# Performance work log

Hardware: AMD Instinct MI355X
Metric: run time of the kernel (lower is better)

## Reference

```python
import jax, jax.numpy as jnp
import numpy as np


def _rnn_scan(x_tbi, h0, Wih, Whh, bih, bhh):
    # x_tbi: [T,B,I], h0: [B,H]. PyTorch nn.RNN cell: h = tanh(x@Wih^T + bih + h@Whh^T + bhh)
    def step(h, xt):
        h_new = jnp.tanh(xt @ Wih.T + bih + h @ Whh.T + bhh)
        return h_new, h_new
    h_last, hs = jax.lax.scan(step, h0, x_tbi)
    return h_last, hs


def setup_inputs() -> dict:
    key = jax.random.key(0)
    ks = jax.random.split(key, 12)
    B, T, I, H, O = 4096, 64, 3, 128, 3
    s = 1.0 / np.sqrt(H)
    d = {
        "x": jax.random.normal(ks[0], (B, T, I), dtype=jnp.float32),
        "enc_Wih": jax.random.uniform(ks[1], (H, I), jnp.float32, -s, s),
        "enc_Whh": jax.random.uniform(ks[2], (H, H), jnp.float32, -s, s),
        "enc_bih": jax.random.uniform(ks[3], (H,), jnp.float32, -s, s),
        "enc_bhh": jax.random.uniform(ks[4], (H,), jnp.float32, -s, s),
        "dec_Wih": jax.random.uniform(ks[5], (H, O), jnp.float32, -s, s),
        "dec_Whh": jax.random.uniform(ks[6], (H, H), jnp.float32, -s, s),
        "dec_bih": jax.random.uniform(ks[7], (H,), jnp.float32, -s, s),
        "dec_bhh": jax.random.uniform(ks[8], (H,), jnp.float32, -s, s),
        "fc_W": jax.random.uniform(ks[9], (O, H), jnp.float32, -s, s),
        "fc_b": jax.random.uniform(ks[10], (O,), jnp.float32, -s, s),
        "pred_len": 32,
    }
    return d


def reference(x, enc_Wih, enc_Whh, enc_bih, enc_bhh,
              dec_Wih, dec_Whh, dec_bih, dec_bhh, fc_W, fc_b, pred_len):
    B, T, _ = x.shape
    H = enc_Whh.shape[0]
    h0 = jnp.zeros((B, H), dtype=x.dtype)
    # Encoder over LOOK_BACK steps
    h, _ = _rnn_scan(jnp.swapaxes(x, 0, 1), h0, enc_Wih, enc_Whh, enc_bih, enc_bhh)
    dec_in0 = x[:, -1, :]  # [B,O]

    def step(carry, _):
        h, inp = carry
        h_new = jnp.tanh(inp @ dec_Wih.T + dec_bih + h @ dec_Whh.T + dec_bhh)
        pred = h_new @ fc_W.T + fc_b
        return (h_new, pred), pred

    _, preds = jax.lax.scan(step, (h, dec_in0), None, length=pred_len)
    out = jnp.swapaxes(preds, 0, 1)  # [B, pred_len, O]
    if pred_len == 1:
        return out[:, 0, :]
    return out
```

## Files before the change

kernel.cpp:

```cpp
#include <hip/hip_runtime.h>

typedef short short8 __attribute__((ext_vector_type(8)));
typedef float f32x4 __attribute__((ext_vector_type(4)));

#define H 128
#define NB 8
#define TSTEPS 64
#define PRED 32
#define XSTRIDE 260


static __device__ __forceinline__ unsigned short bf16_rne(float f) {
  unsigned u = __builtin_bit_cast(unsigned, f);
  u += 0x7fffu + ((u >> 16) & 1u);
  return (unsigned short)(u >> 16);
}
static __device__ __forceinline__ float bf16_f(unsigned short s) {
  unsigned u = ((unsigned)s) << 16;
  return __builtin_bit_cast(float, u);
}
static __device__ __forceinline__ float tanh_fast(float v) {
  v = fminf(9.0f, fmaxf(-9.0f, v));
  float e = __expf(2.0f * v);
  return __fdividef(e - 1.0f, e + 1.0f);
}

static __device__ __forceinline__ void split_frag(const f32x4& a, const f32x4& b,
                                                  short8& hi, short8& lo) {
  #pragma unroll
  for (int e = 0; e < 4; ++e) {
    unsigned short h1 = bf16_rne(a[e]);
    hi[e] = (short)h1;
    lo[e] = (short)bf16_rne(a[e] - bf16_f(h1));
    unsigned short h2 = bf16_rne(b[e]);
    hi[e + 4] = (short)h2;
    lo[e + 4] = (short)bf16_rne(b[e] - bf16_f(h2));
  }
}

__global__ __launch_bounds__(256, 2) void traj_kernel(
    const float* __restrict__ x,
    const float* __restrict__ eWih, const float* __restrict__ eWhh,
    const float* __restrict__ ebih, const float* __restrict__ ebhh,
    const float* __restrict__ dWih, const float* __restrict__ dWhh,
    const float* __restrict__ dbih, const float* __restrict__ dbhh,
    const float* __restrict__ fcW, const float* __restrict__ fcb,
    float* __restrict__ out)
{
  __shared__ __align__(16) float x_lds[16 * XSTRIDE];
  __shared__ __align__(16) short h_hi0[16 * H], h_lo0[16 * H];
  __shared__ __align__(16) short h_hi1[16 * H], h_lo1[16 * H];
  __shared__ float inp_lds[16][4];

  const int tid = threadIdx.x;
  const int lane = tid & 63;
  const int w = tid >> 6;
  const int l4 = lane >> 4;
  const int ln = lane & 15;
  const int r0 = blockIdx.x * NB;
  const int jj0 = w * 32 + ln;
  const int jj1 = jj0 + 16;

  #pragma unroll
  for (int s = 0; s < 12; ++s) {
    int flat = tid + s * 256;
    int r = flat / 192;
    int rem = flat - r * 192;
    int t = rem / 3;
    int i = rem - t * 3;
    int g = (r >> 2) * 2 + (r & 1);
    x_lds[r * XSTRIDE + t * 4 + i] = x[(size_t)(r0 + g) * 192 + rem];
  }
  #pragma unroll
  for (int s = 0; s < 8; ++s) {
    h_hi0[tid + s * 256] = 0; h_hi1[tid + s * 256] = 0;
    h_lo0[tid + s * 256] = 0; h_lo1[tid + s * 256] = 0;
  }

  short8 whi[2][4], wlo[2][4];
  #pragma unroll
  for (int ct = 0; ct < 2; ++ct) {
    const int j = ct ? jj1 : jj0;
    #pragma unroll
    for (int kt = 0; kt < 4; ++kt) {
      const float* p = eWhh + j * H + kt * 32 + l4 * 8;
      split_frag(*(const f32x4*)p, *(const f32x4*)(p + 4), whi[ct][kt], wlo[ct][kt]);
    }
  }
  float bias0 = ebih[jj0] + ebhh[jj0];
  float bias1 = ebih[jj1] + ebhh[jj1];
  float wi0[3], wi1[3];
  #pragma unroll
  for (int i = 0; i < 3; ++i) { wi0[i] = eWih[jj0 * 3 + i]; wi1[i] = eWih[jj1 * 3 + i]; }

  int roff[4];
  #pragma unroll
  for (int kt = 0; kt < 4; ++kt)
    roff[kt] = ln * H + ((((kt << 2) + l4) ^ ln) << 3);
  int wo0[2], wo1[2], xb[2];
  #pragma unroll
  for (int reg = 0; reg < 2; ++reg) {
    const int r = l4 * 4 + reg;
    wo0[reg] = r * H + (((jj0 >> 3) ^ r) << 3) + (jj0 & 7);
    wo1[reg] = r * H + (((jj1 >> 3) ^ r) << 3) + (jj1 & 7);
    xb[reg] = r * XSTRIDE;
  }

  auto load_frags = [&](const short* __restrict__ hh, const short* __restrict__ hl,
                        short8* ah, short8* al) {
    #pragma unroll
    for (int kt = 0; kt < 4; ++kt) {
      ah[kt] = *(const short8*)&hh[roff[kt]];
      al[kt] = *(const short8*)&hl[roff[kt]];
    }
  };
  auto rnn_core = [&](const short8* ah, const short8* al, f32x4 a0, f32x4 a1,
                      short* __restrict__ wh, short* __restrict__ wl) {
    f32x4 b0 = {0.f, 0.f, 0.f, 0.f}, b1 = {0.f, 0.f, 0.f, 0.f};
    f32x4 c0 = {0.f, 0.f, 0.f, 0.f}, c1 = {0.f, 0.f, 0.f, 0.f};
    #pragma unroll
    for (int kt = 0; kt < 4; ++kt) {
      a0 = __builtin_amdgcn_mfma_f32_16x16x32_bf16(ah[kt], whi[0][kt], a0, 0, 0, 0);
      a1 = __builtin_amdgcn_mfma_f32_16x16x32_bf16(ah[kt], whi[1][kt], a1, 0, 0, 0);
      b0 = __builtin_amdgcn_mfma_f32_16x16x32_bf16(ah[kt], wlo[0][kt], b0, 0, 0, 0);
      b1 = __builtin_amdgcn_mfma_f32_16x16x32_bf16(ah[kt], wlo[1][kt], b1, 0, 0, 0);
      c0 = __builtin_amdgcn_mfma_f32_16x16x32_bf16(al[kt], whi[0][kt], c0, 0, 0, 0);
      c1 = __builtin_amdgcn_mfma_f32_16x16x32_bf16(al[kt], whi[1][kt], c1, 0, 0, 0);
    }
    #pragma unroll
    for (int reg = 0; reg < 2; ++reg) {
      float v0 = tanh_fast(a0[reg] + b0[reg] + c0[reg]);
      float v1 = tanh_fast(a1[reg] + b1[reg] + c1[reg]);
      unsigned short p0 = bf16_rne(v0);
      unsigned short p1 = bf16_rne(v1);
      wh[wo0[reg]] = (short)p0;
      wl[wo0[reg]] = (short)bf16_rne(v0 - bf16_f(p0));
      wh[wo1[reg]] = (short)p1;
      wl[wo1[reg]] = (short)bf16_rne(v1 - bf16_f(p1));
    }
  };

  __syncthreads();

  for (int t = 0; t < TSTEPS; t += 2) {
    {
      short8 ah[4], al[4];
      load_frags(h_hi0, h_lo0, ah, al);
      f32x4 a0 = {0.f, 0.f, bias0, bias0}, a1 = {0.f, 0.f, bias1, bias1};
      #pragma unroll
      for (int reg = 0; reg < 2; ++reg) {
        const f32x4 xv = *(const f32x4*)&x_lds[xb[reg] + t * 4];
        a0[reg] = bias0 + wi0[0] * xv[0] + wi0[1] * xv[1] + wi0[2] * xv[2];
        a1[reg] = bias1 + wi1[0] * xv[0] + wi1[1] * xv[1] + wi1[2] * xv[2];
      }
      rnn_core(ah, al, a0, a1, h_hi1, h_lo1);
    }
    __syncthreads();
    {
      short8 ah[4], al[4];
      load_frags(h_hi1, h_lo1, ah, al);
      f32x4 a0 = {0.f, 0.f, bias0, bias0}, a1 = {0.f, 0.f, bias1, bias1};
      #pragma unroll
      for (int reg = 0; reg < 2; ++reg) {
        const f32x4 xv = *(const f32x4*)&x_lds[xb[reg] + (t + 1) * 4];
        a0[reg] = bias0 + wi0[0] * xv[0] + wi0[1] * xv[1] + wi0[2] * xv[2];
        a1[reg] = bias1 + wi1[0] * xv[0] + wi1[1] * xv[1] + wi1[2] * xv[2];
      }
      rnn_core(ah, al, a0, a1, h_hi0, h_lo0);
    }
    __syncthreads();
  }

  #pragma unroll
  for (int ct = 0; ct < 2; ++ct) {
    const int j = ct ? jj1 : jj0;
    #pragma unroll
    for (int kt = 0; kt < 4; ++kt) {
      const float* p = dWhh + j * H + kt * 32 + l4 * 8;
      split_frag(*(const f32x4*)p, *(const f32x4*)(p + 4), whi[ct][kt], wlo[ct][kt]);
    }
  }
  bias0 = dbih[jj0] + dbhh[jj0];
  bias1 = dbih[jj1] + dbhh[jj1];
  #pragma unroll
  for (int i = 0; i < 3; ++i) { wi0[i] = dWih[jj0 * 3 + i]; wi1[i] = dWih[jj1 * 3 + i]; }

  short8 fhi[4];
  #pragma unroll
  for (int kt = 0; kt < 4; ++kt) {
    f32x4 a = {0.f, 0.f, 0.f, 0.f}, b = {0.f, 0.f, 0.f, 0.f};
    if (ln < 3) {
      const float* p = fcW + ln * H + kt * 32 + l4 * 8;
      a = *(const f32x4*)p;
      b = *(const f32x4*)(p + 4);
    }
    short8 hi;
    #pragma unroll
    for (int e = 0; e < 4; ++e) {
      hi[e] = (short)bf16_rne(a[e]);
      hi[e + 4] = (short)bf16_rne(b[e]);
    }
    fhi[kt] = hi;
  }
  const float fcbl = (ln < 3) ? fcb[ln] : 0.f;

  if (tid < 48) {
    int r = tid / 3, i = tid - 3 * (tid / 3);
    inp_lds[r][i] = x_lds[r * XSTRIDE + 63 * 4 + i];
  }
  __syncthreads();

  {
    short8 ah[4], al[4];
    load_frags(h_hi0, h_lo0, ah, al);
    f32x4 a0 = {0.f, 0.f, bias0, bias0}, a1 = {0.f, 0.f, bias1, bias1};
    #pragma unroll
    for (int reg = 0; reg < 2; ++reg) {
      const int r = l4 * 4 + reg;
      a0[reg] = bias0 + wi0[0] * inp_lds[r][0] + wi0[1] * inp_lds[r][1]
                      + wi0[2] * inp_lds[r][2];
      a1[reg] = bias1 + wi1[0] * inp_lds[r][0] + wi1[1] * inp_lds[r][1]
                      + wi1[2] * inp_lds[r][2];
    }
    rnn_core(ah, al, a0, a1, h_hi1, h_lo1);
  }
  __syncthreads();

  #pragma unroll
  for (int ct = 0; ct < 2; ++ct) {
    const int j = ct ? jj1 : jj0;
    const float* wip = ct ? wi1 : wi0;
    #pragma unroll
    for (int kt = 0; kt < 4; ++kt) {
      const int kb = kt * 32 + l4 * 8;
      f32x4 a = *(const f32x4*)(dWhh + j * H + kb);
      f32x4 b = *(const f32x4*)(dWhh + j * H + kb + 4);
      #pragma unroll
      for (int o = 0; o < 3; ++o) {
        const f32x4 fa = *(const f32x4*)(fcW + o * H + kb);
        const f32x4 fb = *(const f32x4*)(fcW + o * H + kb + 4);
        #pragma unroll
        for (int e = 0; e < 4; ++e) {
          a[e] += wip[o] * fa[e];
          b[e] += wip[o] * fb[e];
        }
      }
      split_frag(a, b, whi[ct][kt], wlo[ct][kt]);
    }
  }
  const float biasp0 = bias0 + wi0[0] * fcb[0] + wi0[1] * fcb[1] + wi0[2] * fcb[2];
  const float biasp1 = bias1 + wi1[0] * fcb[0] + wi1[1] * fcb[1] + wi1[2] * fcb[2];
  const f32x4 accd0 = {biasp0, biasp0, biasp0, biasp0};
  const f32x4 accd1 = {biasp1, biasp1, biasp1, biasp1};

  const short* rdh = h_hi1; const short* rdl = h_lo1;
  short* wrh = h_hi0;       short* wrl = h_lo0;
  for (int s = 1; s < PRED; ++s) {
    short8 ah[4], al[4];
    load_frags(rdh, rdl, ah, al);
    rnn_core(ah, al, accd0, accd1, wrh, wrl);
    if (w == (s & 3)) {
      f32x4 p0 = {0.f, 0.f, 0.f, 0.f};
      f32x4 p1 = {0.f, 0.f, 0.f, 0.f};
      #pragma unroll
      for (int kt = 0; kt < 4; ++kt) {
        p0 = __builtin_amdgcn_mfma_f32_16x16x32_bf16(ah[kt], fhi[kt], p0, 0, 0, 0);
        p1 = __builtin_amdgcn_mfma_f32_16x16x32_bf16(al[kt], fhi[kt], p1, 0, 0, 0);
      }
      if (ln < 3) {
        #pragma unroll
        for (int reg = 0; reg < 2; ++reg)
          out[((size_t)(r0 + l4 * 2 + reg) * PRED + (s - 1)) * 3 + ln] =
              p0[reg] + p1[reg] + fcbl;
      }
    }
    __syncthreads();
    const short* th = rdh; rdh = wrh; wrh = (short*)th;
    const short* tl = rdl; rdl = wrl; wrl = (short*)tl;
  }
  if (w == 0) {
    short8 ah[4], al[4];
    load_frags(rdh, rdl, ah, al);
    f32x4 p0 = {0.f, 0.f, 0.f, 0.f};
    f32x4 p1 = {0.f, 0.f, 0.f, 0.f};
    #pragma unroll
    for (int kt = 0; kt < 4; ++kt) {
      p0 = __builtin_amdgcn_mfma_f32_16x16x32_bf16(ah[kt], fhi[kt], p0, 0, 0, 0);
      p1 = __builtin_amdgcn_mfma_f32_16x16x32_bf16(al[kt], fhi[kt], p1, 0, 0, 0);
    }
    if (ln < 3) {
      #pragma unroll
      for (int reg = 0; reg < 2; ++reg)
        out[((size_t)(r0 + l4 * 2 + reg) * PRED + (PRED - 1)) * 3 + ln] =
            p0[reg] + p1[reg] + fcbl;
    }
  }
}

extern "C" void kernel_launch(void* const* d_in, const int* in_sizes, int n_in,
                              void* d_out, int out_size, void* d_ws, size_t ws_size,
                              hipStream_t stream) {
  (void)in_sizes; (void)n_in; (void)out_size; (void)d_ws; (void)ws_size;
  const float* x    = (const float*)d_in[0];
  const float* eWih = (const float*)d_in[1];
  const float* eWhh = (const float*)d_in[2];
  const float* ebih = (const float*)d_in[3];
  const float* ebhh = (const float*)d_in[4];
  const float* dWih = (const float*)d_in[5];
  const float* dWhh = (const float*)d_in[6];
  const float* dbih = (const float*)d_in[7];
  const float* dbhh = (const float*)d_in[8];
  const float* fcW  = (const float*)d_in[9];
  const float* fcb  = (const float*)d_in[10];
  float* out = (float*)d_out;
  traj_kernel<<<dim3(512), dim3(256), 0, stream>>>(
      x, eWih, eWhh, ebih, ebhh, dWih, dWhh, dbih, dbhh, fcW, fcb, out);
}
```

Baseline: 167.0 us.

## Use all 16 MFMA rows per block and stream x from global

New measurement: 166.4 us. About the same (-0.3%).

```diff
diff --git a/kernel.cpp b/kernel.cpp
--- a/kernel.cpp
+++ b/kernel.cpp
@@ -4,10 +4,9 @@
 typedef float f32x4 __attribute__((ext_vector_type(4)));
 
 #define H 128
-#define NB 8
+#define NB 16
 #define TSTEPS 64
 #define PRED 32
-#define XSTRIDE 260
 
 
 static __device__ __forceinline__ unsigned short bf16_rne(float f) {
@@ -38,7 +37,7 @@
   }
 }
 
-__global__ __launch_bounds__(256, 2) void traj_kernel(
+__global__ __launch_bounds__(256, 1) void traj_kernel(
     const float* __restrict__ x,
     const float* __restrict__ eWih, const float* __restrict__ eWhh,
     const float* __restrict__ ebih, const float* __restrict__ ebhh,
@@ -47,10 +46,8 @@
     const float* __restrict__ fcW, const float* __restrict__ fcb,
     float* __restrict__ out)
 {
-  __shared__ __align__(16) float x_lds[16 * XSTRIDE];
-  __shared__ __align__(16) short h_hi0[16 * H], h_lo0[16 * H];
-  __shared__ __align__(16) short h_hi1[16 * H], h_lo1[16 * H];
-  __shared__ float inp_lds[16][4];
+  __shared__ __align__(16) short h_hi0[NB * H], h_lo0[NB * H];
+  __shared__ __align__(16) short h_hi1[NB * H], h_lo1[NB * H];
 
   const int tid = threadIdx.x;
   const int lane = tid & 63;
@@ -58,23 +55,13 @@
   const int l4 = lane >> 4;
   const int ln = lane & 15;
   const int r0 = blockIdx.x * NB;
-  const int jj0 = w * 32 + ln;
-  const int jj1 = jj0 + 16;
-
-  #pragma unroll
-  for (int s = 0; s < 12; ++s) {
-    int flat = tid + s * 256;
-    int r = flat / 192;
-    int rem = flat - r * 192;
-    int t = rem / 3;
-    int i = rem - t * 3;
-    int g = (r >> 2) * 2 + (r & 1);
-    x_lds[r * XSTRIDE + t * 4 + i] = x[(size_t)(r0 + g) * 192 + rem];
-  }
+  const int jj0 = w * 32 + 2 * ln;
+  const int jj1 = jj0 + 1;
+
   #pragma unroll
   for (int s = 0; s < 8; ++s) {
-    h_hi0[tid + s * 256] = 0; h_hi1[tid + s * 256] = 0;
-    h_lo0[tid + s * 256] = 0; h_lo1[tid + s * 256] = 0;
+    h_hi0[tid + s * 256] = 0;
+    h_lo0[tid + s * 256] = 0;
   }
 
   short8 whi[2][4], wlo[2][4];
@@ -97,13 +84,13 @@
   #pragma unroll
   for (int kt = 0; kt < 4; ++kt)
     roff[kt] = ln * H + ((((kt << 2) + l4) ^ ln) << 3);
-  int wo0[2], wo1[2], xb[2];
-  #pragma unroll
-  for (int reg = 0; reg < 2; ++reg) {
+  int wob[4];
+  const float* xrow[4];
+  #pragma unroll
+  for (int reg = 0; reg < 4; ++reg) {
     const int r = l4 * 4 + reg;
-    wo0[reg] = r * H + (((jj0 >> 3) ^ r) << 3) + (jj0 & 7);
-    wo1[reg] = r * H + (((jj1 >> 3) ^ r) << 3) + (jj1 & 7);
-    xb[reg] = r * XSTRIDE;
+    wob[reg] = r * H + (((jj0 >> 3) ^ r) << 3) + (jj0 & 7);
+    xrow[reg] = x + (size_t)(r0 + r) * 192;
   }
 
   auto load_frags = [&](const short* __restrict__ hh, const short* __restrict__ hl,
@@ -128,17 +115,23 @@
       c1 = __builtin_amdgcn_mfma_f32_16x16x32_bf16(al[kt], whi[1][kt], c1, 0, 0, 0);
     }
     #pragma unroll
-    for (int reg = 0; reg < 2; ++reg) {
+    for (int reg = 0; reg < 4; ++reg) {
       float v0 = tanh_fast(a0[reg] + b0[reg] + c0[reg]);
       float v1 = tanh_fast(a1[reg] + b1[reg] + c1[reg]);
       unsigned short p0 = bf16_rne(v0);
       unsigned short p1 = bf16_rne(v1);
-      wh[wo0[reg]] = (short)p0;
-      wl[wo0[reg]] = (short)bf16_rne(v0 - bf16_f(p0));
-      wh[wo1[reg]] = (short)p1;
-      wl[wo1[reg]] = (short)bf16_rne(v1 - bf16_f(p1));
+      unsigned short l0 = bf16_rne(v0 - bf16_f(p0));
+      unsigned short l1 = bf16_rne(v1 - bf16_f(p1));
+      *(unsigned*)&wh[wob[reg]] = (unsigned)p0 | ((unsigned)p1 << 16);
+      *(unsigned*)&wl[wob[reg]] = (unsigned)l0 | ((unsigned)l1 << 16);
     }
   };
+
+  float xc[4][3], xn[4][3];
+  #pragma unroll
+  for (int reg = 0; reg < 4; ++reg)
+    #pragma unroll
+    for (int i = 0; i < 3; ++i) xc[reg][i] = xrow[reg][i];
 
   __syncthreads();
 
@@ -146,29 +139,36 @@
     {
       short8 ah[4], al[4];
       load_frags(h_hi0, h_lo0, ah, al);
-      f32x4 a0 = {0.f, 0.f, bias0, bias0}, a1 = {0.f, 0.f, bias1, bias1};
-      #pragma unroll
-      for (int reg = 0; reg < 2; ++reg) {
-        const f32x4 xv = *(const f32x4*)&x_lds[xb[reg] + t * 4];
-        a0[reg] = bias0 + wi0[0] * xv[0] + wi0[1] * xv[1] + wi0[2] * xv[2];
-        a1[reg] = bias1 + wi1[0] * xv[0] + wi1[1] * xv[1] + wi1[2] * xv[2];
-      }
+      f32x4 a0, a1;
+      #pragma unroll
+      for (int reg = 0; reg < 4; ++reg) {
+        a0[reg] = bias0 + wi0[0] * xc[reg][0] + wi0[1] * xc[reg][1] + wi0[2] * xc[reg][2];
+        a1[reg] = bias1 + wi1[0] * xc[reg][0] + wi1[1] * xc[reg][1] + wi1[2] * xc[reg][2];
+      }
+      #pragma unroll
+      for (int reg = 0; reg < 4; ++reg)
+        #pragma unroll
+        for (int i = 0; i < 3; ++i) xn[reg][i] = xrow[reg][(t + 1) * 3 + i];
       rnn_core(ah, al, a0, a1, h_hi1, h_lo1);
-    }
-    __syncthreads();
+      __syncthreads();
+    }
     {
       short8 ah[4], al[4];
       load_frags(h_hi1, h_lo1, ah, al);
-      f32x4 a0 = {0.f, 0.f, bias0, bias0}, a1 = {0.f, 0.f, bias1, bias1};
-      #pragma unroll
-      for (int reg = 0; reg < 2; ++reg) {
-        const f32x4 xv = *(const f32x4*)&x_lds[xb[reg] + (t + 1) * 4];
-        a0[reg] = bias0 + wi0[0] * xv[0] + wi0[1] * xv[1] + wi0[2] * xv[2];
-        a1[reg] = bias1 + wi1[0] * xv[0] + wi1[1] * xv[1] + wi1[2] * xv[2];
-      }
+      f32x4 a0, a1;
+      #pragma unroll
+      for (int reg = 0; reg < 4; ++reg) {
+        a0[reg] = bias0 + wi0[0] * xn[reg][0] + wi0[1] * xn[reg][1] + wi0[2] * xn[reg][2];
+        a1[reg] = bias1 + wi1[0] * xn[reg][0] + wi1[1] * xn[reg][1] + wi1[2] * xn[reg][2];
+      }
+      const int tp = (t + 2 < TSTEPS) ? (t + 2) : (TSTEPS - 1);
+      #pragma unroll
+      for (int reg = 0; reg < 4; ++reg)
+        #pragma unroll
+        for (int i = 0; i < 3; ++i) xc[reg][i] = xrow[reg][tp * 3 + i];
       rnn_core(ah, al, a0, a1, h_hi0, h_lo0);
-    }
-    __syncthreads();
+      __syncthreads();
+    }
   }
 
   #pragma unroll
@@ -204,23 +204,14 @@
   }
   const float fcbl = (ln < 3) ? fcb[ln] : 0.f;
 
-  if (tid < 48) {
-    int r = tid / 3, i = tid - 3 * (tid / 3);
-    inp_lds[r][i] = x_lds[r * XSTRIDE + 63 * 4 + i];
-  }
-  __syncthreads();
-
   {
     short8 ah[4], al[4];
     load_frags(h_hi0, h_lo0, ah, al);
-    f32x4 a0 = {0.f, 0.f, bias0, bias0}, a1 = {0.f, 0.f, bias1, bias1};
-    #pragma unroll
-    for (int reg = 0; reg < 2; ++reg) {
-      const int r = l4 * 4 + reg;
-      a0[reg] = bias0 + wi0[0] * inp_lds[r][0] + wi0[1] * inp_lds[r][1]
-                      + wi0[2] * inp_lds[r][2];
-      a1[reg] = bias1 + wi1[0] * inp_lds[r][0] + wi1[1] * inp_lds[r][1]
-                      + wi1[2] * inp_lds[r][2];
+    f32x4 a0, a1;
+    #pragma unroll
+    for (int reg = 0; reg < 4; ++reg) {
+      a0[reg] = bias0 + wi0[0] * xc[reg][0] + wi0[1] * xc[reg][1] + wi0[2] * xc[reg][2];
+      a1[reg] = bias1 + wi1[0] * xc[reg][0] + wi1[1] * xc[reg][1] + wi1[2] * xc[reg][2];
     }
     rnn_core(ah, al, a0, a1, h_hi1, h_lo1);
   }
@@ -269,8 +260,8 @@
       }
       if (ln < 3) {
         #pragma unroll
-        for (int reg = 0; reg < 2; ++reg)
-          out[((size_t)(r0 + l4 * 2 + reg) * PRED + (s - 1)) * 3 + ln] =
+        for (int reg = 0; reg < 4; ++reg)
+          out[((size_t)(r0 + l4 * 4 + reg) * PRED + (s - 1)) * 3 + ln] =
               p0[reg] + p1[reg] + fcbl;
       }
     }
@@ -290,8 +281,8 @@
     }
     if (ln < 3) {
       #pragma unroll
-      for (int reg = 0; reg < 2; ++reg)
-        out[((size_t)(r0 + l4 * 2 + reg) * PRED + (PRED - 1)) * 3 + ln] =
+      for (int reg = 0; reg < 4; ++reg)
+        out[((size_t)(r0 + l4 * 4 + reg) * PRED + (PRED - 1)) * 3 + ln] =
             p0[reg] + p1[reg] + fcbl;
     }
   }
@@ -313,6 +304,6 @@
   const float* fcW  = (const float*)d_in[9];
   const float* fcb  = (const float*)d_in[10];
   float* out = (float*)d_out;
-  traj_kernel<<<dim3(512), dim3(256), 0, stream>>>(
+  traj_kernel<<<dim3(256), dim3(256), 0, stream>>>(
       x, eWih, eWhh, ebih, ebhh, dWih, dWhh, dbih, dbhh, fcW, fcb, out);
 }
```
